# Kernel optimization log

Measured on AMD Instinct MI355X. Metric: run time of the kernel, lower is better.

Reference implementation:

```python
import jax, jax.numpy as jnp
import numpy as np

HIDDEN = 512
NUM_HEADS = 8
ATTN_DIM = HIDDEN // NUM_HEADS  # 64
B, S = 2, 2048
MASK_FILL = -1e9


def setup_inputs() -> dict:
    key = jax.random.key(0)
    ks = jax.random.split(key, 16)
    scale = HIDDEN ** -0.5
    inp = {
        'q': jax.random.normal(ks[0], (B, S, HIDDEN), jnp.float32),
        'k': jax.random.normal(ks[1], (B, S, HIDDEN), jnp.float32),
        'v': jax.random.normal(ks[2], (B, S, HIDDEN), jnp.float32),
        'attn_bias': jax.random.normal(ks[3], (B, NUM_HEADS, S, S), jnp.float32),
        'attn_mask': jax.random.bernoulli(ks[4], 0.1, (B, S, S)),  # True = masked
        # Linear weights stored as [in, out] (= torch weight.T), biases [out]
        'Wq': jax.random.normal(ks[5], (HIDDEN, HIDDEN), jnp.float32) * scale,
        'bq': jax.random.normal(ks[6], (HIDDEN,), jnp.float32) * 0.02,
        'Wk': jax.random.normal(ks[7], (HIDDEN, HIDDEN), jnp.float32) * scale,
        'bk': jax.random.normal(ks[8], (HIDDEN,), jnp.float32) * 0.02,
        'Wv': jax.random.normal(ks[9], (HIDDEN, HIDDEN), jnp.float32) * scale,
        'bv': jax.random.normal(ks[10], (HIDDEN,), jnp.float32) * 0.02,
        'Wo': jax.random.normal(ks[11], (HIDDEN, HIDDEN), jnp.float32) * scale,
        'bo': jax.random.normal(ks[12], (HIDDEN,), jnp.float32) * 0.02,
    }
    return inp


def reference(q, k, v, attn_bias, attn_mask, Wq, bq, Wk, bk, Wv, bv, Wo, bo):
    b, s, _ = q.shape
    H, D = NUM_HEADS, ATTN_DIM
    qh = (q @ Wq + bq).reshape(b, s, H, D)   # [B,S,H,D]
    kh = (k @ Wk + bk).reshape(b, -1, H, D)
    vh = (v @ Wv + bv).reshape(b, -1, H, D)
    # scaled dot-product scores [B,H,Sq,Sk]
    x = jnp.einsum('bqhd,bkhd->bhqk', qh, kh) * (D ** -0.5)
    x = x + attn_bias
    x = jnp.where(attn_mask[:, None, :, :], MASK_FILL, x)
    attention_scores = jax.nn.softmax(x, axis=-1)
    # dropout is identity in eval mode
    ctx = jnp.einsum('bhqk,bkhd->bqhd', attention_scores, vh).reshape(b, s, H * D)
    out = ctx @ Wo + bo
    return out, attention_scores
```

## Files before the change

kernel.cpp:

```cpp
#include <hip/hip_runtime.h>
#include <hip/hip_bf16.h>

constexpr int HID = 512;
constexpr int NH  = 8;
constexpr int HD  = 64;
constexpr int NB  = 2;
constexpr int SEQ = 2048;
constexpr int M   = NB * SEQ;
constexpr int NROWS = NB * NH * SEQ;
constexpr int SKB = SEQ / 64;
constexpr int PVSPLIT = 2;

typedef __attribute__((ext_vector_type(8))) short bf16x8;
typedef __attribute__((ext_vector_type(4))) float f32x4;

__device__ __forceinline__ unsigned short f2bf(float x){
    union { float f; unsigned u; } v; v.f = x;
    return (unsigned short)((v.u + 0x7fffu + ((v.u >> 16) & 1u)) >> 16);
}
__device__ __forceinline__ float bf2f(unsigned short h){
    union { unsigned u; float f; } v; v.u = (unsigned)h << 16;
    return v.f;
}

__global__ void cvt_split(const float* __restrict__ x, unsigned short* __restrict__ hi,
                          unsigned short* __restrict__ lo, int n){
    int i = blockIdx.x * 256 + threadIdx.x;
    if (i >= n) return;
    float f = x[i];
    unsigned short h = f2bf(f);
    hi[i] = h;
    if (lo) lo[i] = f2bf(f - bf2f(h));
}

__global__ void cvt_w(const float* __restrict__ w, unsigned short* __restrict__ hi,
                      unsigned short* __restrict__ lo){
    __shared__ float t[32][33];
    int n0 = blockIdx.x * 32, k0 = blockIdx.y * 32;
    int tx = threadIdx.x, ty = threadIdx.y;
    for (int r = ty; r < 32; r += 8)
        t[r][tx] = w[(size_t)(k0 + r) * HID + n0 + tx];
    __syncthreads();
    for (int r = ty; r < 32; r += 8){
        float f = t[tx][r];
        unsigned short hb = f2bf(f);
        size_t o = (size_t)(n0 + r) * HID + k0 + tx;
        hi[o] = hb;
        if (lo) lo[o] = f2bf(f - bf2f(hb));
    }
}

template<int SPLIT, int VOUT>
__global__ __launch_bounds__(256) void proj_gemm(
    const unsigned short* __restrict__ Ahi, const unsigned short* __restrict__ Alo,
    const unsigned short* __restrict__ Bhi, const unsigned short* __restrict__ Blo,
    const float* __restrict__ bias,
    unsigned short* __restrict__ Ohi, unsigned short* __restrict__ Olo)
{
    __shared__ __align__(16) unsigned short As[SPLIT + 1][64][40];
    __shared__ __align__(16) unsigned short Bs[SPLIT + 1][64][40];
    const int m0 = blockIdx.y * 64, n0 = blockIdx.x * 64;
    const int tid = threadIdx.x, w = tid >> 6, lane = tid & 63;
    const int wm = (w >> 1) * 32, wn = (w & 1) * 32;
    const int srow = tid >> 2, sch = (tid & 3) * 8;
    f32x4 acc[2][2] = {};
    for (int k0 = 0; k0 < HID; k0 += 32){
        *(bf16x8*)&As[0][srow][sch] = *(const bf16x8*)(Ahi + (size_t)(m0 + srow) * HID + k0 + sch);
        *(bf16x8*)&Bs[0][srow][sch] = *(const bf16x8*)(Bhi + (size_t)(n0 + srow) * HID + k0 + sch);
        if (SPLIT){
            *(bf16x8*)&As[1][srow][sch] = *(const bf16x8*)(Alo + (size_t)(m0 + srow) * HID + k0 + sch);
            *(bf16x8*)&Bs[1][srow][sch] = *(const bf16x8*)(Blo + (size_t)(n0 + srow) * HID + k0 + sch);
        }
        __syncthreads();
        const int fr = lane & 15, kc = (lane >> 4) * 8;
        #pragma unroll
        for (int fm = 0; fm < 2; fm++)
        #pragma unroll
        for (int fn = 0; fn < 2; fn++){
            bf16x8 aH = *(bf16x8*)&As[0][wm + fm*16 + fr][kc];
            bf16x8 bH = *(bf16x8*)&Bs[0][wn + fn*16 + fr][kc];
            acc[fm][fn] = __builtin_amdgcn_mfma_f32_16x16x32_bf16(aH, bH, acc[fm][fn], 0, 0, 0);
            if (SPLIT){
                bf16x8 aL = *(bf16x8*)&As[1][wm + fm*16 + fr][kc];
                bf16x8 bL = *(bf16x8*)&Bs[1][wn + fn*16 + fr][kc];
                acc[fm][fn] = __builtin_amdgcn_mfma_f32_16x16x32_bf16(aL, bH, acc[fm][fn], 0, 0, 0);
                acc[fm][fn] = __builtin_amdgcn_mfma_f32_16x16x32_bf16(aH, bL, acc[fm][fn], 0, 0, 0);
            }
        }
        __syncthreads();
    }
    #pragma unroll
    for (int fm = 0; fm < 2; fm++)
    #pragma unroll
    for (int fn = 0; fn < 2; fn++){
        int col = n0 + wn + fn*16 + (lane & 15);
        int rb  = m0 + wm + fm*16 + (lane >> 4) * 4;
        float bv = bias[col];
        int h = col >> 6, d = col & 63;
        #pragma unroll
        for (int e = 0; e < 4; e++){
            int m = rb + e;
            int b = m >> 11, s = m & (SEQ - 1);
            float y = acc[fm][fn][e] + bv;
            if (VOUT){
                Ohi[((size_t)((b * NH + h) * HD + d)) * SEQ + s] = f2bf(y);
            } else {
                size_t o = ((size_t)((b * NH + h) * SEQ + s)) * HD + d;
                unsigned short hb = f2bf(y);
                Ohi[o] = hb;
                if (SPLIT) Olo[o] = f2bf(y - bf2f(hb));
            }
        }
    }
}

__global__ __launch_bounds__(256) void scores_kernel(
    const unsigned short* __restrict__ qh_hi, const unsigned short* __restrict__ qh_lo,
    const unsigned short* __restrict__ kh_hi, const unsigned short* __restrict__ kh_lo,
    const float* __restrict__ attn_bias, const int* __restrict__ attn_mask,
    float* __restrict__ scores, float* __restrict__ partials)
{
    __shared__ union {
        struct { unsigned short Aq[2][64][72]; unsigned short Bk[2][64][72]; } s;
        float Pt[64][68];
    } u;
    __shared__ float rs[64][4];
    const int bh = blockIdx.x, sk0 = blockIdx.y * 64, sq0 = blockIdx.z * 64;
    const int b = bh >> 3;
    const int tid = threadIdx.x, w = tid >> 6, lane = tid & 63;
    const int wm = (w >> 1) * 32, wn = (w & 1) * 32;

    for (int idx = tid; idx < 512; idx += 256){
        int row = idx >> 3, ch = (idx & 7) * 8;
        size_t qo = ((size_t)bh * SEQ + sq0 + row) * HD + ch;
        size_t ko = ((size_t)bh * SEQ + sk0 + row) * HD + ch;
        *(bf16x8*)&u.s.Aq[0][row][ch] = *(const bf16x8*)(qh_hi + qo);
        *(bf16x8*)&u.s.Aq[1][row][ch] = *(const bf16x8*)(qh_lo + qo);
        *(bf16x8*)&u.s.Bk[0][row][ch] = *(const bf16x8*)(kh_hi + ko);
        *(bf16x8*)&u.s.Bk[1][row][ch] = *(const bf16x8*)(kh_lo + ko);
    }
    __syncthreads();
    f32x4 acc[2][2] = {};
    const int fr = lane & 15, kc8 = (lane >> 4) * 8;
    #pragma unroll
    for (int ks = 0; ks < 2; ks++){
        int kc = ks * 32 + kc8;
        #pragma unroll
        for (int fm = 0; fm < 2; fm++)
        #pragma unroll
        for (int fn = 0; fn < 2; fn++){
            bf16x8 aH = *(bf16x8*)&u.s.Aq[0][wm + fm*16 + fr][kc];
            bf16x8 aL = *(bf16x8*)&u.s.Aq[1][wm + fm*16 + fr][kc];
            bf16x8 bH = *(bf16x8*)&u.s.Bk[0][wn + fn*16 + fr][kc];
            bf16x8 bL = *(bf16x8*)&u.s.Bk[1][wn + fn*16 + fr][kc];
            acc[fm][fn] = __builtin_amdgcn_mfma_f32_16x16x32_bf16(aH, bH, acc[fm][fn], 0, 0, 0);
            acc[fm][fn] = __builtin_amdgcn_mfma_f32_16x16x32_bf16(aL, bH, acc[fm][fn], 0, 0, 0);
            acc[fm][fn] = __builtin_amdgcn_mfma_f32_16x16x32_bf16(aH, bL, acc[fm][fn], 0, 0, 0);
        }
    }
    __syncthreads();
    #pragma unroll
    for (int fm = 0; fm < 2; fm++)
    #pragma unroll
    for (int fn = 0; fn < 2; fn++){
        int c  = wn + fn*16 + (lane & 15);
        int rb = wm + fm*16 + (lane >> 4) * 4;
        #pragma unroll
        for (int e = 0; e < 4; e++)
            u.Pt[rb + e][c] = acc[fm][fn][e] * 0.125f;
    }
    __syncthreads();
    {
        const int r = tid >> 2, qq = tid & 3;
        const size_t rowoff = ((size_t)bh * SEQ + sq0 + r) * SEQ + sk0 + qq * 16;
        const float* brow = attn_bias + rowoff;
        const int*   mrow = attn_mask + ((size_t)(b * SEQ + sq0 + r)) * SEQ + sk0 + qq * 16;
        float*       srow = scores + rowoff;
        float sum = 0.f;
        #pragma unroll
        for (int j = 0; j < 4; j++){
            float4 bi = *(const float4*)(brow + j * 4);
            int4   mk = *(const int4*)(mrow + j * 4);
            float4 xv = *(const float4*)&u.Pt[r][qq * 16 + j * 4];
            float4 pv;
            pv.x = mk.x ? 0.f : __expf(xv.x + bi.x);
            pv.y = mk.y ? 0.f : __expf(xv.y + bi.y);
            pv.z = mk.z ? 0.f : __expf(xv.z + bi.z);
            pv.w = mk.w ? 0.f : __expf(xv.w + bi.w);
            *(float4*)(srow + j * 4) = pv;
            sum += pv.x + pv.y + pv.z + pv.w;
        }
        rs[r][qq] = sum;
    }
    __syncthreads();
    if (tid < 64){
        float s = rs[tid][0] + rs[tid][1] + rs[tid][2] + rs[tid][3];
        partials[(size_t)blockIdx.y * NROWS + (size_t)bh * SEQ + sq0 + tid] = s;
    }
}

__global__ void rowsum_inv(const float* __restrict__ partials, float* __restrict__ invl){
    int r = blockIdx.x * 256 + threadIdx.x;
    float s = 0.f;
    for (int j = 0; j < SKB; j++) s += partials[(size_t)j * NROWS + r];
    invl[r] = 1.0f / s;
}

__global__ __launch_bounds__(256) void pv_kernel(
    float* __restrict__ scores, const float* __restrict__ invl,
    const unsigned short* __restrict__ vh_t, float* __restrict__ ctx_part)
{
    __shared__ __align__(16) unsigned short Ap[64][72];
    __shared__ __align__(16) unsigned short Bv[64][72];
    __shared__ float il[64];
    const int sq0 = blockIdx.x * 64, bh = blockIdx.y, sp = blockIdx.z;
    const int tid = threadIdx.x, w = tid >> 6, lane = tid & 63;
    const int wm = (w >> 1) * 32, wn = (w & 1) * 32;
    if (tid < 64) il[tid] = invl[(size_t)bh * SEQ + sq0 + tid];
    __syncthreads();
    f32x4 acc[2][2] = {};
    const int skbeg = sp * (SEQ / PVSPLIT), skend = skbeg + SEQ / PVSPLIT;
    for (int sk0 = skbeg; sk0 < skend; sk0 += 64){
        for (int idx = tid; idx < 1024; idx += 256){
            int row = idx >> 4, c4 = (idx & 15) * 4;
            size_t o = ((size_t)bh * SEQ + sq0 + row) * SEQ + sk0 + c4;
            float4 pv = *(float4*)(scores + o);
            float sc = il[row];
            pv.x *= sc; pv.y *= sc; pv.z *= sc; pv.w *= sc;
            *(float4*)(scores + o) = pv;
            ushort4 u; u.x = f2bf(pv.x); u.y = f2bf(pv.y); u.z = f2bf(pv.z); u.w = f2bf(pv.w);
            *(ushort4*)&Ap[row][c4] = u;
        }
        for (int idx = tid; idx < 512; idx += 256){
            int row = idx >> 3, ch = (idx & 7) * 8;
            *(bf16x8*)&Bv[row][ch] = *(const bf16x8*)(vh_t + ((size_t)bh * HD + row) * SEQ + sk0 + ch);
        }
        __syncthreads();
        const int fr = lane & 15, kc8 = (lane >> 4) * 8;
        #pragma unroll
        for (int ks = 0; ks < 2; ks++){
            int kc = ks * 32 + kc8;
            #pragma unroll
            for (int fm = 0; fm < 2; fm++)
            #pragma unroll
            for (int fn = 0; fn < 2; fn++){
                bf16x8 a  = *(bf16x8*)&Ap[wm + fm*16 + fr][kc];
                bf16x8 bb = *(bf16x8*)&Bv[wn + fn*16 + fr][kc];
                acc[fm][fn] = __builtin_amdgcn_mfma_f32_16x16x32_bf16(a, bb, acc[fm][fn], 0, 0, 0);
            }
        }
        __syncthreads();
    }
    #pragma unroll
    for (int fm = 0; fm < 2; fm++)
    #pragma unroll
    for (int fn = 0; fn < 2; fn++){
        int c  = wn + fn*16 + (lane & 15);
        int rb = wm + fm*16 + (lane >> 4) * 4;
        #pragma unroll
        for (int e = 0; e < 4; e++)
            ctx_part[((size_t)sp * NROWS + (size_t)bh * SEQ + sq0 + rb + e) * HD + c] = acc[fm][fn][e];
    }
}

__global__ void ctx_reduce(const float* __restrict__ part, unsigned short* __restrict__ ctx){
    int i = blockIdx.x * 256 + threadIdx.x;
    float s = 0.f;
    #pragma unroll
    for (int sp = 0; sp < PVSPLIT; sp++) s += part[(size_t)sp * NROWS * HD + i];
    int m = i >> 6, d = i & 63;
    int bhv = m >> 11, s_ = m & (SEQ - 1);
    int b = bhv >> 3, h = bhv & 7;
    ctx[((size_t)(b * SEQ + s_)) * HID + h * HD + d] = f2bf(s);
}

__global__ __launch_bounds__(256) void out_gemm(
    const unsigned short* __restrict__ A, const unsigned short* __restrict__ Bt,
    const float* __restrict__ bias, float* __restrict__ out)
{
    __shared__ __align__(16) unsigned short As[64][40];
    __shared__ __align__(16) unsigned short Bs[64][40];
    const int m0 = blockIdx.y * 64, n0 = blockIdx.x * 64;
    const int tid = threadIdx.x, w = tid >> 6, lane = tid & 63;
    const int wm = (w >> 1) * 32, wn = (w & 1) * 32;
    const int srow = tid >> 2, sch = (tid & 3) * 8;
    f32x4 acc[2][2] = {};
    for (int k0 = 0; k0 < HID; k0 += 32){
        *(bf16x8*)&As[srow][sch] = *(const bf16x8*)(A  + (size_t)(m0 + srow) * HID + k0 + sch);
        *(bf16x8*)&Bs[srow][sch] = *(const bf16x8*)(Bt + (size_t)(n0 + srow) * HID + k0 + sch);
        __syncthreads();
        const int fr = lane & 15, kc = (lane >> 4) * 8;
        #pragma unroll
        for (int fm = 0; fm < 2; fm++)
        #pragma unroll
        for (int fn = 0; fn < 2; fn++){
            bf16x8 a = *(bf16x8*)&As[wm + fm*16 + fr][kc];
            bf16x8 b = *(bf16x8*)&Bs[wn + fn*16 + fr][kc];
            acc[fm][fn] = __builtin_amdgcn_mfma_f32_16x16x32_bf16(a, b, acc[fm][fn], 0, 0, 0);
        }
        __syncthreads();
    }
    #pragma unroll
    for (int fm = 0; fm < 2; fm++)
    #pragma unroll
    for (int fn = 0; fn < 2; fn++){
        int col = n0 + wn + fn*16 + (lane & 15);
        int rb  = m0 + wm + fm*16 + (lane >> 4) * 4;
        float bv = bias[col];
        #pragma unroll
        for (int e = 0; e < 4; e++)
            out[(size_t)(rb + e) * HID + col] = acc[fm][fn][e] + bv;
    }
}

extern "C" void kernel_launch(void* const* d_in, const int* in_sizes, int n_in,
                              void* d_out, int out_size, void* d_ws, size_t ws_size,
                              hipStream_t stream)
{
    const float* q  = (const float*)d_in[0];
    const float* k  = (const float*)d_in[1];
    const float* v  = (const float*)d_in[2];
    const float* attn_bias = (const float*)d_in[3];
    const int*   attn_mask = (const int*)d_in[4];
    const float* Wq = (const float*)d_in[5];
    const float* bq = (const float*)d_in[6];
    const float* Wk = (const float*)d_in[7];
    const float* bk = (const float*)d_in[8];
    const float* Wv = (const float*)d_in[9];
    const float* bv = (const float*)d_in[10];
    const float* Wo = (const float*)d_in[11];
    const float* bo = (const float*)d_in[12];

    float* out = (float*)d_out;
    float* scores = out + (size_t)M * HID;

    char* p = (char*)d_ws;
    auto alloc = [&](size_t bytes){ char* r = p; p += (bytes + 255) & ~(size_t)255; return r; };
    const size_t PLANE  = (size_t)M * HID * 2;
    const size_t WPLANE = (size_t)HID * HID * 2;
    unsigned short* q_hi = (unsigned short*)alloc(PLANE);
    unsigned short* q_lo = (unsigned short*)alloc(PLANE);
    unsigned short* k_hi = (unsigned short*)alloc(PLANE);
    unsigned short* k_lo = (unsigned short*)alloc(PLANE);
    unsigned short* v_b  = (unsigned short*)alloc(PLANE);
    unsigned short* wqt_hi = (unsigned short*)alloc(WPLANE);
    unsigned short* wqt_lo = (unsigned short*)alloc(WPLANE);
    unsigned short* wkt_hi = (unsigned short*)alloc(WPLANE);
    unsigned short* wkt_lo = (unsigned short*)alloc(WPLANE);
    unsigned short* wvt    = (unsigned short*)alloc(WPLANE);
    unsigned short* wot    = (unsigned short*)alloc(WPLANE);
    unsigned short* qh_hi = (unsigned short*)alloc(PLANE);
    unsigned short* qh_lo = (unsigned short*)alloc(PLANE);
    unsigned short* kh_hi = (unsigned short*)alloc(PLANE);
    unsigned short* kh_lo = (unsigned short*)alloc(PLANE);
    unsigned short* vh_t  = (unsigned short*)alloc(PLANE);
    unsigned short* ctx   = (unsigned short*)alloc(PLANE);
    float* partials = (float*)alloc((size_t)SKB * NROWS * 4);
    float* invl     = (float*)alloc((size_t)NROWS * 4);
    if ((size_t)(p - (char*)d_ws) > ws_size) return;
    float* ctx_part = (float*)q_hi;

    const int n = M * HID;
    cvt_split<<<(n + 255) / 256, 256, 0, stream>>>(q, q_hi, q_lo, n);
    cvt_split<<<(n + 255) / 256, 256, 0, stream>>>(k, k_hi, k_lo, n);
    cvt_split<<<(n + 255) / 256, 256, 0, stream>>>(v, v_b, nullptr, n);
    dim3 wb(32, 8);
    cvt_w<<<dim3(16, 16), wb, 0, stream>>>(Wq, wqt_hi, wqt_lo);
    cvt_w<<<dim3(16, 16), wb, 0, stream>>>(Wk, wkt_hi, wkt_lo);
    cvt_w<<<dim3(16, 16), wb, 0, stream>>>(Wv, wvt, nullptr);
    cvt_w<<<dim3(16, 16), wb, 0, stream>>>(Wo, wot, nullptr);

    dim3 pg(HID / 64, M / 64);
    proj_gemm<1,0><<<pg, 256, 0, stream>>>(q_hi, q_lo, wqt_hi, wqt_lo, bq, qh_hi, qh_lo);
    proj_gemm<1,0><<<pg, 256, 0, stream>>>(k_hi, k_lo, wkt_hi, wkt_lo, bk, kh_hi, kh_lo);
    proj_gemm<0,1><<<pg, 256, 0, stream>>>(v_b, nullptr, wvt, nullptr, bv, vh_t, nullptr);

    scores_kernel<<<dim3(NB * NH, SKB, SEQ / 64), 256, 0, stream>>>(
        qh_hi, qh_lo, kh_hi, kh_lo, attn_bias, attn_mask, scores, partials);
    rowsum_inv<<<NROWS / 256, 256, 0, stream>>>(partials, invl);
    pv_kernel<<<dim3(SEQ / 64, NB * NH, PVSPLIT), 256, 0, stream>>>(scores, invl, vh_t, ctx_part);
    ctx_reduce<<<(NROWS * HD) / 256, 256, 0, stream>>>(ctx_part, ctx);
    out_gemm<<<dim3(HID / 64, M / 64), 256, 0, stream>>>(ctx, wot, bo, out);
}
```

Before: 868.0 us.

## Fuse scores, softmax normalization and PV into one two-pass attention kernel

Replaces the scores kernel, rowsum kernel, split PV kernel and context reduction with one kernel per 64-query tile. A first pass over all keys computes row sums of exp(scores+bias); a second pass recomputes QK, writes normalized probabilities and accumulates P·V directly into bf16 context. This removes the read-modify-write of the full score matrix and three launches, at the cost of reading bias and mask twice, recomputing QK, narrower uncoalesced scalar loads, and fewer blocks.

```diff
diff --git a/kernel.cpp b/kernel.cpp
--- a/kernel.cpp
+++ b/kernel.cpp
@@ -8,8 +8,6 @@
 constexpr int SEQ = 2048;
 constexpr int M   = NB * SEQ;
 constexpr int NROWS = NB * NH * SEQ;
-constexpr int SKB = SEQ / 64;
-constexpr int PVSPLIT = 2;
 
 typedef __attribute__((ext_vector_type(8))) short bf16x8;
 typedef __attribute__((ext_vector_type(4))) float f32x4;
@@ -114,164 +112,159 @@
     }
 }
 
-__global__ __launch_bounds__(256) void scores_kernel(
+__global__ __launch_bounds__(512, 4) void attn_fused(
     const unsigned short* __restrict__ qh_hi, const unsigned short* __restrict__ qh_lo,
     const unsigned short* __restrict__ kh_hi, const unsigned short* __restrict__ kh_lo,
+    const unsigned short* __restrict__ vh_t,
     const float* __restrict__ attn_bias, const int* __restrict__ attn_mask,
-    float* __restrict__ scores, float* __restrict__ partials)
+    float* __restrict__ scores, unsigned short* __restrict__ ctx)
 {
-    __shared__ union {
-        struct { unsigned short Aq[2][64][72]; unsigned short Bk[2][64][72]; } s;
-        float Pt[64][68];
-    } u;
+    __shared__ __align__(16) unsigned short Ks[2][64][72];
+    __shared__ __align__(16) unsigned short Vs[64][72];
+    __shared__ __align__(16) unsigned short Ps[64][72];
     __shared__ float rs[64][4];
-    const int bh = blockIdx.x, sk0 = blockIdx.y * 64, sq0 = blockIdx.z * 64;
-    const int b = bh >> 3;
-    const int tid = threadIdx.x, w = tid >> 6, lane = tid & 63;
-    const int wm = (w >> 1) * 32, wn = (w & 1) * 32;
-
-    for (int idx = tid; idx < 512; idx += 256){
-        int row = idx >> 3, ch = (idx & 7) * 8;
-        size_t qo = ((size_t)bh * SEQ + sq0 + row) * HD + ch;
-        size_t ko = ((size_t)bh * SEQ + sk0 + row) * HD + ch;
-        *(bf16x8*)&u.s.Aq[0][row][ch] = *(const bf16x8*)(qh_hi + qo);
-        *(bf16x8*)&u.s.Aq[1][row][ch] = *(const bf16x8*)(qh_lo + qo);
-        *(bf16x8*)&u.s.Bk[0][row][ch] = *(const bf16x8*)(kh_hi + ko);
-        *(bf16x8*)&u.s.Bk[1][row][ch] = *(const bf16x8*)(kh_lo + ko);
+    __shared__ float il[64];
+
+    const int sq0 = blockIdx.x * 64;
+    const int bh  = blockIdx.y;
+    const int b   = bh >> 3, h = bh & 7;
+    const int tid = threadIdx.x;
+    const int w   = tid >> 6, lane = tid & 63;
+    const int wv  = w >> 2;
+    const int wn  = (w & 3) * 16;
+    const int fr  = lane & 15, lg = lane >> 4;
+    const int kc8 = lg * 8;
+    const int srow = tid >> 3, sch = (tid & 7) * 8;
+
+    bf16x8 qHf[2][2], qLf[2][2];
+    #pragma unroll
+    for (int fm = 0; fm < 2; fm++){
+        size_t qrow = ((size_t)bh * SEQ + sq0 + wv*32 + fm*16 + fr) * HD;
+        #pragma unroll
+        for (int ks = 0; ks < 2; ks++){
+            qHf[fm][ks] = *(const bf16x8*)(qh_hi + qrow + ks*32 + kc8);
+            qLf[fm][ks] = *(const bf16x8*)(qh_lo + qrow + ks*32 + kc8);
+        }
+    }
+
+    float rsum[2][4] = {};
+    for (int sk0 = 0; sk0 < SEQ; sk0 += 64){
+        {
+            size_t koff = ((size_t)bh * SEQ + sk0 + srow) * HD + sch;
+            *(bf16x8*)&Ks[0][srow][sch] = *(const bf16x8*)(kh_hi + koff);
+            *(bf16x8*)&Ks[1][srow][sch] = *(const bf16x8*)(kh_lo + koff);
+        }
+        __syncthreads();
+        f32x4 acc[2] = {};
+        #pragma unroll
+        for (int ks = 0; ks < 2; ks++){
+            bf16x8 bH = *(bf16x8*)&Ks[0][wn + fr][ks*32 + kc8];
+            bf16x8 bL = *(bf16x8*)&Ks[1][wn + fr][ks*32 + kc8];
+            #pragma unroll
+            for (int fm = 0; fm < 2; fm++){
+                acc[fm] = __builtin_amdgcn_mfma_f32_16x16x32_bf16(qHf[fm][ks], bH, acc[fm], 0, 0, 0);
+                acc[fm] = __builtin_amdgcn_mfma_f32_16x16x32_bf16(qLf[fm][ks], bH, acc[fm], 0, 0, 0);
+                acc[fm] = __builtin_amdgcn_mfma_f32_16x16x32_bf16(qHf[fm][ks], bL, acc[fm], 0, 0, 0);
+            }
+        }
+        #pragma unroll
+        for (int fm = 0; fm < 2; fm++){
+            int row = sq0 + wv*32 + fm*16 + lg*4;
+            const float* bp = attn_bias + ((size_t)bh * SEQ + row) * SEQ + sk0 + wn + fr;
+            const int*   mp = attn_mask + ((size_t)b  * SEQ + row) * SEQ + sk0 + wn + fr;
+            #pragma unroll
+            for (int e = 0; e < 4; e++){
+                float bv = bp[(size_t)e * SEQ];
+                int   mv = mp[(size_t)e * SEQ];
+                float p = mv ? 0.f : __expf(acc[fm][e] * 0.125f + bv);
+                rsum[fm][e] += p;
+            }
+        }
+        __syncthreads();
+    }
+    #pragma unroll
+    for (int m = 1; m < 16; m <<= 1)
+        #pragma unroll
+        for (int fm = 0; fm < 2; fm++)
+            #pragma unroll
+            for (int e = 0; e < 4; e++)
+                rsum[fm][e] += __shfl_xor(rsum[fm][e], m, 64);
+    if (fr == 0){
+        #pragma unroll
+        for (int fm = 0; fm < 2; fm++)
+            #pragma unroll
+            for (int e = 0; e < 4; e++)
+                rs[wv*32 + fm*16 + lg*4 + e][w & 3] = rsum[fm][e];
     }
     __syncthreads();
-    f32x4 acc[2][2] = {};
-    const int fr = lane & 15, kc8 = (lane >> 4) * 8;
-    #pragma unroll
-    for (int ks = 0; ks < 2; ks++){
-        int kc = ks * 32 + kc8;
-        #pragma unroll
-        for (int fm = 0; fm < 2; fm++)
-        #pragma unroll
-        for (int fn = 0; fn < 2; fn++){
-            bf16x8 aH = *(bf16x8*)&u.s.Aq[0][wm + fm*16 + fr][kc];
-            bf16x8 aL = *(bf16x8*)&u.s.Aq[1][wm + fm*16 + fr][kc];
-            bf16x8 bH = *(bf16x8*)&u.s.Bk[0][wn + fn*16 + fr][kc];
-            bf16x8 bL = *(bf16x8*)&u.s.Bk[1][wn + fn*16 + fr][kc];
-            acc[fm][fn] = __builtin_amdgcn_mfma_f32_16x16x32_bf16(aH, bH, acc[fm][fn], 0, 0, 0);
-            acc[fm][fn] = __builtin_amdgcn_mfma_f32_16x16x32_bf16(aL, bH, acc[fm][fn], 0, 0, 0);
-            acc[fm][fn] = __builtin_amdgcn_mfma_f32_16x16x32_bf16(aH, bL, acc[fm][fn], 0, 0, 0);
-        }
-    }
+    if (tid < 64) il[tid] = 1.0f / (rs[tid][0] + rs[tid][1] + rs[tid][2] + rs[tid][3]);
     __syncthreads();
+    float ilv[2][4];
     #pragma unroll
     for (int fm = 0; fm < 2; fm++)
-    #pragma unroll
-    for (int fn = 0; fn < 2; fn++){
-        int c  = wn + fn*16 + (lane & 15);
-        int rb = wm + fm*16 + (lane >> 4) * 4;
         #pragma unroll
         for (int e = 0; e < 4; e++)
-            u.Pt[rb + e][c] = acc[fm][fn][e] * 0.125f;
-    }
+            ilv[fm][e] = il[wv*32 + fm*16 + lg*4 + e];
+
+    f32x4 cacc[2] = {};
+    for (int sk0 = 0; sk0 < SEQ; sk0 += 64){
+        {
+            size_t koff = ((size_t)bh * SEQ + sk0 + srow) * HD + sch;
+            *(bf16x8*)&Ks[0][srow][sch] = *(const bf16x8*)(kh_hi + koff);
+            *(bf16x8*)&Ks[1][srow][sch] = *(const bf16x8*)(kh_lo + koff);
+            *(bf16x8*)&Vs[srow][sch]    = *(const bf16x8*)(vh_t + ((size_t)bh * HD + srow) * SEQ + sk0 + sch);
+        }
+        __syncthreads();
+        f32x4 acc[2] = {};
+        #pragma unroll
+        for (int ks = 0; ks < 2; ks++){
+            bf16x8 bH = *(bf16x8*)&Ks[0][wn + fr][ks*32 + kc8];
+            bf16x8 bL = *(bf16x8*)&Ks[1][wn + fr][ks*32 + kc8];
+            #pragma unroll
+            for (int fm = 0; fm < 2; fm++){
+                acc[fm] = __builtin_amdgcn_mfma_f32_16x16x32_bf16(qHf[fm][ks], bH, acc[fm], 0, 0, 0);
+                acc[fm] = __builtin_amdgcn_mfma_f32_16x16x32_bf16(qLf[fm][ks], bH, acc[fm], 0, 0, 0);
+                acc[fm] = __builtin_amdgcn_mfma_f32_16x16x32_bf16(qHf[fm][ks], bL, acc[fm], 0, 0, 0);
+            }
+        }
+        #pragma unroll
+        for (int fm = 0; fm < 2; fm++){
+            int row = sq0 + wv*32 + fm*16 + lg*4;
+            const float* bp = attn_bias + ((size_t)bh * SEQ + row) * SEQ + sk0 + wn + fr;
+            const int*   mp = attn_mask + ((size_t)b  * SEQ + row) * SEQ + sk0 + wn + fr;
+            float*       sp = scores    + ((size_t)bh * SEQ + row) * SEQ + sk0 + wn + fr;
+            #pragma unroll
+            for (int e = 0; e < 4; e++){
+                float bv = bp[(size_t)e * SEQ];
+                int   mv = mp[(size_t)e * SEQ];
+                float p = mv ? 0.f : __expf(acc[fm][e] * 0.125f + bv);
+                float pn = p * ilv[fm][e];
+                sp[(size_t)e * SEQ] = pn;
+                Ps[wv*32 + fm*16 + lg*4 + e][wn + fr] = f2bf(pn);
+            }
+        }
+        __syncthreads();
+        #pragma unroll
+        for (int ks = 0; ks < 2; ks++){
+            bf16x8 bV = *(bf16x8*)&Vs[wn + fr][ks*32 + kc8];
+            #pragma unroll
+            for (int fm = 0; fm < 2; fm++){
+                bf16x8 a = *(bf16x8*)&Ps[wv*32 + fm*16 + fr][ks*32 + kc8];
+                cacc[fm] = __builtin_amdgcn_mfma_f32_16x16x32_bf16(a, bV, cacc[fm], 0, 0, 0);
+            }
+        }
+        __syncthreads();
+    }
+    #pragma unroll
+    for (int fm = 0; fm < 2; fm++)
+        #pragma unroll
+        for (int e = 0; e < 4; e++)
+            Ps[wv*32 + fm*16 + lg*4 + e][wn + fr] = f2bf(cacc[fm][e]);
     __syncthreads();
     {
-        const int r = tid >> 2, qq = tid & 3;
-        const size_t rowoff = ((size_t)bh * SEQ + sq0 + r) * SEQ + sk0 + qq * 16;
-        const float* brow = attn_bias + rowoff;
-        const int*   mrow = attn_mask + ((size_t)(b * SEQ + sq0 + r)) * SEQ + sk0 + qq * 16;
-        float*       srow = scores + rowoff;
-        float sum = 0.f;
-        #pragma unroll
-        for (int j = 0; j < 4; j++){
-            float4 bi = *(const float4*)(brow + j * 4);
-            int4   mk = *(const int4*)(mrow + j * 4);
-            float4 xv = *(const float4*)&u.Pt[r][qq * 16 + j * 4];
-            float4 pv;
-            pv.x = mk.x ? 0.f : __expf(xv.x + bi.x);
-            pv.y = mk.y ? 0.f : __expf(xv.y + bi.y);
-            pv.z = mk.z ? 0.f : __expf(xv.z + bi.z);
-            pv.w = mk.w ? 0.f : __expf(xv.w + bi.w);
-            *(float4*)(srow + j * 4) = pv;
-            sum += pv.x + pv.y + pv.z + pv.w;
-        }
-        rs[r][qq] = sum;
-    }
-    __syncthreads();
-    if (tid < 64){
-        float s = rs[tid][0] + rs[tid][1] + rs[tid][2] + rs[tid][3];
-        partials[(size_t)blockIdx.y * NROWS + (size_t)bh * SEQ + sq0 + tid] = s;
-    }
-}
-
-__global__ void rowsum_inv(const float* __restrict__ partials, float* __restrict__ invl){
-    int r = blockIdx.x * 256 + threadIdx.x;
-    float s = 0.f;
-    for (int j = 0; j < SKB; j++) s += partials[(size_t)j * NROWS + r];
-    invl[r] = 1.0f / s;
-}
-
-__global__ __launch_bounds__(256) void pv_kernel(
-    float* __restrict__ scores, const float* __restrict__ invl,
-    const unsigned short* __restrict__ vh_t, float* __restrict__ ctx_part)
-{
-    __shared__ __align__(16) unsigned short Ap[64][72];
-    __shared__ __align__(16) unsigned short Bv[64][72];
-    __shared__ float il[64];
-    const int sq0 = blockIdx.x * 64, bh = blockIdx.y, sp = blockIdx.z;
-    const int tid = threadIdx.x, w = tid >> 6, lane = tid & 63;
-    const int wm = (w >> 1) * 32, wn = (w & 1) * 32;
-    if (tid < 64) il[tid] = invl[(size_t)bh * SEQ + sq0 + tid];
-    __syncthreads();
-    f32x4 acc[2][2] = {};
-    const int skbeg = sp * (SEQ / PVSPLIT), skend = skbeg + SEQ / PVSPLIT;
-    for (int sk0 = skbeg; sk0 < skend; sk0 += 64){
-        for (int idx = tid; idx < 1024; idx += 256){
-            int row = idx >> 4, c4 = (idx & 15) * 4;
-            size_t o = ((size_t)bh * SEQ + sq0 + row) * SEQ + sk0 + c4;
-            float4 pv = *(float4*)(scores + o);
-            float sc = il[row];
-            pv.x *= sc; pv.y *= sc; pv.z *= sc; pv.w *= sc;
-            *(float4*)(scores + o) = pv;
-            ushort4 u; u.x = f2bf(pv.x); u.y = f2bf(pv.y); u.z = f2bf(pv.z); u.w = f2bf(pv.w);
-            *(ushort4*)&Ap[row][c4] = u;
-        }
-        for (int idx = tid; idx < 512; idx += 256){
-            int row = idx >> 3, ch = (idx & 7) * 8;
-            *(bf16x8*)&Bv[row][ch] = *(const bf16x8*)(vh_t + ((size_t)bh * HD + row) * SEQ + sk0 + ch);
-        }
-        __syncthreads();
-        const int fr = lane & 15, kc8 = (lane >> 4) * 8;
-        #pragma unroll
-        for (int ks = 0; ks < 2; ks++){
-            int kc = ks * 32 + kc8;
-            #pragma unroll
-            for (int fm = 0; fm < 2; fm++)
-            #pragma unroll
-            for (int fn = 0; fn < 2; fn++){
-                bf16x8 a  = *(bf16x8*)&Ap[wm + fm*16 + fr][kc];
-                bf16x8 bb = *(bf16x8*)&Bv[wn + fn*16 + fr][kc];
-                acc[fm][fn] = __builtin_amdgcn_mfma_f32_16x16x32_bf16(a, bb, acc[fm][fn], 0, 0, 0);
-            }
-        }
-        __syncthreads();
-    }
-    #pragma unroll
-    for (int fm = 0; fm < 2; fm++)
-    #pragma unroll
-    for (int fn = 0; fn < 2; fn++){
-        int c  = wn + fn*16 + (lane & 15);
-        int rb = wm + fm*16 + (lane >> 4) * 4;
-        #pragma unroll
-        for (int e = 0; e < 4; e++)
-            ctx_part[((size_t)sp * NROWS + (size_t)bh * SEQ + sq0 + rb + e) * HD + c] = acc[fm][fn][e];
-    }
-}
-
-__global__ void ctx_reduce(const float* __restrict__ part, unsigned short* __restrict__ ctx){
-    int i = blockIdx.x * 256 + threadIdx.x;
-    float s = 0.f;
-    #pragma unroll
-    for (int sp = 0; sp < PVSPLIT; sp++) s += part[(size_t)sp * NROWS * HD + i];
-    int m = i >> 6, d = i & 63;
-    int bhv = m >> 11, s_ = m & (SEQ - 1);
-    int b = bhv >> 3, h = bhv & 7;
-    ctx[((size_t)(b * SEQ + s_)) * HID + h * HD + d] = f2bf(s);
+        bf16x8 v = *(bf16x8*)&Ps[srow][sch];
+        *(bf16x8*)(ctx + ((size_t)(b * SEQ + sq0 + srow)) * HID + h * HD + sch) = v;
+    }
 }
 
 __global__ __launch_bounds__(256) void out_gemm(
@@ -355,10 +348,7 @@
     unsigned short* kh_lo = (unsigned short*)alloc(PLANE);
     unsigned short* vh_t  = (unsigned short*)alloc(PLANE);
     unsigned short* ctx   = (unsigned short*)alloc(PLANE);
-    float* partials = (float*)alloc((size_t)SKB * NROWS * 4);
-    float* invl     = (float*)alloc((size_t)NROWS * 4);
     if ((size_t)(p - (char*)d_ws) > ws_size) return;
-    float* ctx_part = (float*)q_hi;
 
     const int n = M * HID;
     cvt_split<<<(n + 255) / 256, 256, 0, stream>>>(q, q_hi, q_lo, n);
@@ -375,10 +365,8 @@
     proj_gemm<1,0><<<pg, 256, 0, stream>>>(k_hi, k_lo, wkt_hi, wkt_lo, bk, kh_hi, kh_lo);
     proj_gemm<0,1><<<pg, 256, 0, stream>>>(v_b, nullptr, wvt, nullptr, bv, vh_t, nullptr);
 
-    scores_kernel<<<dim3(NB * NH, SKB, SEQ / 64), 256, 0, stream>>>(
-        qh_hi, qh_lo, kh_hi, kh_lo, attn_bias, attn_mask, scores, partials);
-    rowsum_inv<<<NROWS / 256, 256, 0, stream>>>(partials, invl);
-    pv_kernel<<<dim3(SEQ / 64, NB * NH, PVSPLIT), 256, 0, stream>>>(scores, invl, vh_t, ctx_part);
-    ctx_reduce<<<(NROWS * HD) / 256, 256, 0, stream>>>(ctx_part, ctx);
+    attn_fused<<<dim3(SEQ / 64, NB * NH), 512, 0, stream>>>(
+        qh_hi, qh_lo, kh_hi, kh_lo, vh_t, attn_bias, attn_mask, scores, ctx);
+
     out_gemm<<<dim3(HID / 64, M / 64), 256, 0, stream>>>(ctx, wot, bo, out);
 }
```

After: 1.033 ms. +19.0%, slower.
